# Optimization experiments

Hardware: AMD Instinct MI355X
Metric: run time of the kernel (lower is better)

## Reference

```python
import jax, jax.numpy as jnp
import numpy as np

EMBED_DIM = 1024
NUM_HEADS = 16
HEAD_DIM = EMBED_DIM // NUM_HEADS
EPS = 1e-5


def setup_inputs() -> dict:
    key = jax.random.key(0)
    ks = jax.random.split(key, 7)
    B, S, D = 4, 2048, EMBED_DIM
    s = 1.0 / np.sqrt(D)
    return {
        "x": jax.random.normal(ks[0], (B, S, D), dtype=jnp.float32),
        "W_qkv": jax.random.uniform(ks[1], (D, 3 * D), jnp.float32, -s, s),
        "b_qkv": jax.random.uniform(ks[2], (3 * D,), jnp.float32, -s, s),
        "W_out": jax.random.uniform(ks[3], (D, D), jnp.float32, -s, s),
        "b_out": jax.random.uniform(ks[4], (D,), jnp.float32, -s, s),
        "gamma": jnp.ones((D,), jnp.float32),
        "beta": jnp.zeros((D,), jnp.float32),
    }


def _layer_norm(y, gamma, beta):
    mu = jnp.mean(y, axis=-1, keepdims=True)
    var = jnp.mean(jnp.square(y - mu), axis=-1, keepdims=True)
    return (y - mu) * jax.lax.rsqrt(var + EPS) * gamma + beta


def reference(x, W_qkv, b_qkv, W_out, b_out, gamma, beta):
    B, S, D = x.shape
    H, Hd = NUM_HEADS, HEAD_DIM
    qkv = x @ W_qkv + b_qkv                       # [B,S,3D]
    q, k, v = jnp.split(qkv, 3, axis=-1)
    q = q.reshape(B, S, H, Hd).transpose(0, 2, 1, 3)  # [B,H,S,Hd]
    k = k.reshape(B, S, H, Hd).transpose(0, 2, 1, 3)
    v = v.reshape(B, S, H, Hd).transpose(0, 2, 1, 3)
    scale = 1.0 / np.sqrt(Hd)
    scores = jnp.einsum("bhsd,bhtd->bhst", q, k) * scale  # [B,H,S,S]
    attn = jax.nn.softmax(scores, axis=-1)
    ctx = jnp.einsum("bhst,bhtd->bhsd", attn, v)  # [B,H,S,Hd]
    ctx = ctx.transpose(0, 2, 1, 3).reshape(B, S, D)
    out = ctx @ W_out + b_out
    return _layer_norm(out + x, gamma, beta)
```

## Files before the change

kernel.cpp:

```cpp
#include <hip/hip_runtime.h>
#include <stdint.h>
#include <stddef.h>


#define SEQ    2048
#define DMODEL 1024
#define NHEAD  16
#define HDIM   64

typedef __attribute__((ext_vector_type(4))) float f32x4;
typedef __attribute__((ext_vector_type(16))) float f32x16;
typedef __attribute__((ext_vector_type(8))) short bf16x8;
typedef __attribute__((ext_vector_type(2))) unsigned uint2v;

static __device__ __forceinline__ unsigned short f2b(float f) {
  union { float f; unsigned u; } c; c.f = f;
  unsigned r = c.u + 0x7FFFu + ((c.u >> 16) & 1u);
  return (unsigned short)(r >> 16);
}
static __device__ __forceinline__ unsigned pkbf(float lo, float hi_) {
  unsigned r;
  asm("v_cvt_pk_bf16_f32 %0, %1, %2" : "=v"(r) : "v"(lo), "v"(hi_));
  return r;
}
static __device__ __forceinline__ float exp2v(float x) {
  return __builtin_amdgcn_exp2f(x);
}
static __device__ __forceinline__ uint2v swap32(unsigned a, unsigned b) {
  return __builtin_amdgcn_permlane32_swap(a, b, false, false);
}
static __device__ __forceinline__ void gl_lds16(const void* g, void* l) {
  __builtin_amdgcn_global_load_lds((const __attribute__((address_space(1))) void*)g,
                                   (__attribute__((address_space(3))) void*)l, 16, 0, 0);
}
static __device__ __forceinline__ int swz(int row, int col) {
  return (row * 64 + col) ^ ((row & 7) << 3);
}

__global__ __launch_bounds__(256) void k_prep(const float* __restrict__ Wqkv,
                                              const float* __restrict__ Wout,
                                              const float* __restrict__ X,
                                              unsigned short* __restrict__ wqkvT,
                                              unsigned short* __restrict__ woutT,
                                              unsigned short* __restrict__ Xb) {
  __shared__ unsigned short tile[32][33];
  const int bid = blockIdx.x;
  const int t = threadIdx.x;
  if (bid < 4096) {
    const float* in; unsigned short* out; int C, bx, by;
    if (bid < 3072) { in = Wqkv; out = wqkvT; C = 3072; bx = bid % 96; by = bid / 96; }
    else { int b2 = bid - 3072; in = Wout; out = woutT; C = 1024; bx = b2 & 31; by = b2 >> 5; }
    const int R = 1024;
    const int c0 = bx * 32, r0 = by * 32;
    const int tx = t & 31, ty = t >> 5;
#pragma unroll
    for (int j = 0; j < 4; j++) {
      int rr = ty + j * 8;
      tile[rr][tx] = f2b(in[(size_t)(r0 + rr) * C + c0 + tx]);
    }
    __syncthreads();
#pragma unroll
    for (int j = 0; j < 4; j++) {
      int rr = ty + j * 8;
      out[(size_t)(c0 + rr) * R + r0 + tx] = tile[tx][rr];
    }
  } else {
    const size_t i = ((size_t)(bid - 4096) * 256 + t) * 8;
    f32x4 a = *(const f32x4*)&X[i];
    f32x4 b = *(const f32x4*)&X[i + 4];
    bf16x8 o;
    o[0] = (short)f2b(a[0]); o[1] = (short)f2b(a[1]);
    o[2] = (short)f2b(a[2]); o[3] = (short)f2b(a[3]);
    o[4] = (short)f2b(b[0]); o[5] = (short)f2b(b[1]);
    o[6] = (short)f2b(b[2]); o[7] = (short)f2b(b[3]);
    *(bf16x8*)&Xb[i] = o;
  }
}

__global__ __launch_bounds__(256) void k_gemm_qkv(const unsigned short* __restrict__ X,
                                                  const unsigned short* __restrict__ WT,
                                                  const float* __restrict__ bias,
                                                  unsigned short* __restrict__ qb,
                                                  unsigned short* __restrict__ kb,
                                                  unsigned short* __restrict__ vt) {
  __shared__ __align__(16) unsigned short As[128 * 32];
  __shared__ __align__(16) unsigned short Bs[128 * 32];
  const int t = threadIdx.x;
  const int w = t >> 6, l = t & 63, g = l >> 4, r = l & 15;
  const int wr = w >> 1, wc = w & 1;
  const int bm = blockIdx.x * 128;
  const int bn = blockIdx.y * 128;

  f32x4 acc[4][4];
#pragma unroll
  for (int a = 0; a < 4; a++)
#pragma unroll
    for (int b = 0; b < 4; b++) acc[a][b] = f32x4{0.f, 0.f, 0.f, 0.f};

  for (int k0 = 0; k0 < DMODEL; k0 += 32) {
    __syncthreads();
#pragma unroll
    for (int j = 0; j < 2; j++) {
      int idx = t + j * 256;
      int row = idx >> 2, kc = idx & 3;
      gl_lds16(X + (size_t)(bm + row) * DMODEL + k0 + kc * 8, (char*)As + idx * 16);
      gl_lds16(WT + (size_t)(bn + row) * DMODEL + k0 + kc * 8, (char*)Bs + idx * 16);
    }
    __syncthreads();
    bf16x8 af[4], bf[4];
#pragma unroll
    for (int mf = 0; mf < 4; mf++)
      af[mf] = *(const bf16x8*)&As[(wr * 64 + mf * 16 + r) * 32 + g * 8];
#pragma unroll
    for (int nf = 0; nf < 4; nf++)
      bf[nf] = *(const bf16x8*)&Bs[(wc * 64 + nf * 16 + r) * 32 + g * 8];
#pragma unroll
    for (int mf = 0; mf < 4; mf++)
#pragma unroll
      for (int nf = 0; nf < 4; nf++)
        acc[mf][nf] = __builtin_amdgcn_mfma_f32_16x16x32_bf16(af[mf], bf[nf], acc[mf][nf], 0, 0, 0);
  }

  if (blockIdx.y >= 16) {
    __syncthreads();
    const int bi = bm >> 11, sbase = bm & 2047;
    const int h  = ((bn - 2048) >> 6) + wc;
    const int bh = bi * NHEAD + h;
    unsigned short* Ls = (w < 2) ? (As + w * 2048) : (Bs + (w - 2) * 2048);
#pragma unroll
    for (int p = 0; p < 2; p++) {
#pragma unroll
      for (int nfp = 0; nfp < 2; nfp++)
#pragma unroll
        for (int mf = 0; mf < 4; mf++)
#pragma unroll
          for (int i = 0; i < 4; i++) {
            const int nf = 2 * p + nfp;
            const int dd = nfp * 16 + r;
            const int ss = mf * 16 + g * 4 + i;
            float v = acc[mf][nf][i] + bias[bn + wc * 64 + nf * 16 + r];
            Ls[dd * 64 + (((ss >> 3) ^ (dd & 7)) * 8) + (ss & 7)] = f2b(v);
          }
#pragma unroll
      for (int j = 0; j < 4; j++) {
        const int dd = l >> 1;
        const int ch = (l & 1) * 4 + j;
        bf16x8 ov = *(const bf16x8*)&Ls[dd * 64 + ((ch ^ (dd & 7)) * 8)];
        *(bf16x8*)&vt[((size_t)bh * HDIM + 32 * p + dd) * SEQ + sbase + wr * 64 + ch * 8] = ov;
      }
    }
  } else {
#pragma unroll
    for (int mf = 0; mf < 4; mf++)
#pragma unroll
      for (int nf = 0; nf < 4; nf++)
#pragma unroll
        for (int i = 0; i < 4; i++) {
          int m = bm + wr * 64 + mf * 16 + g * 4 + i;
          int n = bn + wc * 64 + nf * 16 + r;
          float v = acc[mf][nf][i] + bias[n];
          int part = n >> 10, rem = n & 1023, h = rem >> 6, d = rem & 63;
          int bi = m >> 11, s = m & 2047;
          int bh = bi * NHEAD + h;
          if (part == 0)      qb[((size_t)bh * SEQ + s) * HDIM + d] = f2b(v * 0.18033688f);
          else                kb[((size_t)bh * SEQ + s) * HDIM + d] = f2b(v);
        }
  }
}

__global__ __launch_bounds__(256) void k_attn(const unsigned short* __restrict__ qb,
                                              const unsigned short* __restrict__ kb,
                                              const unsigned short* __restrict__ vt,
                                              unsigned short* __restrict__ ctx) {
  __shared__ __align__(16) unsigned short Qs[128 * 64];
  __shared__ __align__(16) unsigned short K0[64 * 64];
  __shared__ __align__(16) unsigned short V0[64 * 64];
  const int t = threadIdx.x;
  const int w = t >> 6, l = t & 63;
  const int ql = l & 31, hi = l >> 5;
  const int bid = blockIdx.x;
  const int xcd = bid & 7;
  const int j_  = bid >> 3;
  const int bh  = xcd * 8 + (j_ >> 4);
  const int q0  = (j_ & 15) * 128;
  const size_t qoff = ((size_t)bh * SEQ + q0) * HDIM;

#pragma unroll
  for (int j = 0; j < 4; j++) {
    int idx = t + j * 256;
    int row = idx >> 3, s = idx & 7;
    gl_lds16(qb + qoff + (size_t)row * 64 + (s ^ (row & 7)) * 8, (char*)Qs + idx * 16);
  }
#pragma unroll
  for (int j = 0; j < 2; j++) {
    int idx = t + j * 256;
    int row = idx >> 3, s = idx & 7;
    gl_lds16(kb + ((size_t)bh * SEQ + row) * HDIM + (s ^ (row & 7)) * 8, (char*)K0 + idx * 16);
    gl_lds16(vt + ((size_t)bh * HDIM + row) * SEQ + (s ^ (row & 7)) * 8, (char*)V0 + idx * 16);
  }
  asm volatile("s_waitcnt vmcnt(4)" ::: "memory");
  __builtin_amdgcn_sched_barrier(0);
  __builtin_amdgcn_s_barrier();

  bf16x8 qf[4];
#pragma unroll
  for (int ds = 0; ds < 4; ds++)
    qf[ds] = *(const bf16x8*)&Qs[swz(w * 32 + ql, ds * 16 + hi * 8)];
  asm volatile("s_waitcnt lgkmcnt(0)" ::: "memory");
  __builtin_amdgcn_sched_barrier(0);
  __builtin_amdgcn_s_barrier();

  bf16x8 ones;
#pragma unroll
  for (int i = 0; i < 8; i++) ones[i] = (short)0x3F80;

  f32x16 acc_o[2];
  f32x16 acc_l;
#pragma unroll
  for (int db = 0; db < 2; db++)
#pragma unroll
    for (int i = 0; i < 16; i++) acc_o[db][i] = 0.f;
#pragma unroll
  for (int i = 0; i < 16; i++) acc_l[i] = 0.f;

  for (int it = 0; it < SEQ / 64; ++it) {
    const int b = it & 1;
    if (it + 1 < SEQ / 64) {
      const int kt = (it + 1) * 64;
      unsigned short* Kd = (b ^ 1) ? Qs : K0;
      unsigned short* Vd = (b ^ 1) ? (Qs + 4096) : V0;
#pragma unroll
      for (int j = 0; j < 2; j++) {
        int idx = t + j * 256;
        int row = idx >> 3, s = idx & 7;
        gl_lds16(kb + ((size_t)bh * SEQ + kt + row) * HDIM + (s ^ (row & 7)) * 8,
                 (char*)Kd + idx * 16);
        gl_lds16(vt + ((size_t)bh * HDIM + row) * SEQ + kt + (s ^ (row & 7)) * 8,
                 (char*)Vd + idx * 16);
      }
      asm volatile("s_waitcnt vmcnt(4)" ::: "memory");
    } else {
      asm volatile("s_waitcnt vmcnt(0)" ::: "memory");
    }
    __builtin_amdgcn_sched_barrier(0);
    __builtin_amdgcn_s_barrier();

    const unsigned short* Kb = b ? Qs : K0;
    const unsigned short* Vb = b ? (Qs + 4096) : V0;

    bf16x8 kf[2][4];
#pragma unroll
    for (int kb2 = 0; kb2 < 2; kb2++)
#pragma unroll
      for (int ds = 0; ds < 4; ds++)
        kf[kb2][ds] = *(const bf16x8*)&Kb[swz(kb2 * 32 + ql, ds * 16 + hi * 8)];

    f32x16 accs[2];
#pragma unroll
    for (int kb2 = 0; kb2 < 2; kb2++)
#pragma unroll
      for (int i = 0; i < 16; i++) accs[kb2][i] = 0.f;
    __builtin_amdgcn_s_setprio(1);
#pragma unroll
    for (int ds = 0; ds < 4; ds++)
#pragma unroll
      for (int kb2 = 0; kb2 < 2; kb2++)
        accs[kb2] = __builtin_amdgcn_mfma_f32_32x32x16_bf16(kf[kb2][ds], qf[ds], accs[kb2], 0, 0, 0);
    __builtin_amdgcn_s_setprio(0);

#pragma unroll
    for (int kb2 = 0; kb2 < 2; kb2++)
#pragma unroll
      for (int i = 0; i < 16; i++) accs[kb2][i] = exp2v(accs[kb2][i]);

    bf16x8 pa[4];
#pragma unroll
    for (int ks = 0; ks < 4; ks++) {
      const int kb2 = ks >> 1, rb = (ks & 1) * 8;
      unsigned wA0 = pkbf(accs[kb2][rb + 0], accs[kb2][rb + 1]);
      unsigned wA1 = pkbf(accs[kb2][rb + 2], accs[kb2][rb + 3]);
      unsigned wB0 = pkbf(accs[kb2][rb + 4], accs[kb2][rb + 5]);
      unsigned wB1 = pkbf(accs[kb2][rb + 6], accs[kb2][rb + 7]);
      uint2v s0 = swap32(wB0, wA0);
      uint2v s1 = swap32(wB1, wA1);
      union { bf16x8 v; unsigned u[4]; } fr;
      fr.u[0] = s0[1]; fr.u[1] = s1[1]; fr.u[2] = s0[0]; fr.u[3] = s1[0];
      pa[ks] = fr.v;
    }

    bf16x8 vf[2][4];
#pragma unroll
    for (int db = 0; db < 2; db++)
#pragma unroll
      for (int ks = 0; ks < 4; ks++)
        vf[db][ks] = *(const bf16x8*)&Vb[swz(db * 32 + ql, ks * 16 + hi * 8)];

    __builtin_amdgcn_s_setprio(1);
#pragma unroll
    for (int ks = 0; ks < 4; ks++) {
#pragma unroll
      for (int db = 0; db < 2; db++)
        acc_o[db] = __builtin_amdgcn_mfma_f32_32x32x16_bf16(vf[db][ks], pa[ks], acc_o[db], 0, 0, 0);
      acc_l = __builtin_amdgcn_mfma_f32_32x32x16_bf16(ones, pa[ks], acc_l, 0, 0, 0);
    }
    __builtin_amdgcn_s_setprio(0);

    __builtin_amdgcn_s_barrier();
  }

  const int bi = bh >> 4, h = bh & 15;
  const float rl = 1.f / acc_l[0];
  unsigned short* Ls = Qs + w * 2048;
#pragma unroll
  for (int db = 0; db < 2; db++)
#pragma unroll
    for (int j = 0; j < 8; j++) {
      const int d0 = db * 32 + (j & 1) * 2 + (j >> 1) * 8 + hi * 4;
      *(unsigned*)&Ls[(ql * 64 + d0) ^ ((ql & 7) << 3)] =
          pkbf(acc_o[db][2 * j] * rl, acc_o[db][2 * j + 1] * rl);
    }
#pragma unroll
  for (int rq = 0; rq < 4; rq++) {
    const int q = rq * 8 + (l >> 3);
    const int c8 = l & 7;
    bf16x8 ov = *(const bf16x8*)&Ls[(q * 64 + c8 * 8) ^ ((q & 7) << 3)];
    *(bf16x8*)&ctx[((size_t)bi * SEQ + q0 + w * 32 + q) * DMODEL + h * 64 + c8 * 8] = ov;
  }
}

__global__ __launch_bounds__(256) void k_gemm_out(const unsigned short* __restrict__ A,
                                                  const unsigned short* __restrict__ WT,
                                                  const float* __restrict__ bias,
                                                  const float* __restrict__ X,
                                                  float* __restrict__ Y) {
  __shared__ __align__(16) unsigned short As[128 * 32];
  __shared__ __align__(16) unsigned short Bs[128 * 32];
  const int t = threadIdx.x;
  const int w = t >> 6, l = t & 63, g = l >> 4, r = l & 15;
  const int wr = w >> 1, wc = w & 1;
  const int bm = blockIdx.x * 128;
  const int bn = blockIdx.y * 128;

  f32x4 acc[4][4];
#pragma unroll
  for (int a = 0; a < 4; a++)
#pragma unroll
    for (int b = 0; b < 4; b++) acc[a][b] = f32x4{0.f, 0.f, 0.f, 0.f};

  for (int k0 = 0; k0 < DMODEL; k0 += 32) {
    __syncthreads();
#pragma unroll
    for (int j = 0; j < 2; j++) {
      int idx = t + j * 256;
      int row = idx >> 2, kc = idx & 3;
      gl_lds16(A + (size_t)(bm + row) * DMODEL + k0 + kc * 8, (char*)As + idx * 16);
      gl_lds16(WT + (size_t)(bn + row) * DMODEL + k0 + kc * 8, (char*)Bs + idx * 16);
    }
    __syncthreads();
    bf16x8 af[4], bf[4];
#pragma unroll
    for (int mf = 0; mf < 4; mf++)
      af[mf] = *(const bf16x8*)&As[(wr * 64 + mf * 16 + r) * 32 + g * 8];
#pragma unroll
    for (int nf = 0; nf < 4; nf++)
      bf[nf] = *(const bf16x8*)&Bs[(wc * 64 + nf * 16 + r) * 32 + g * 8];
#pragma unroll
    for (int mf = 0; mf < 4; mf++)
#pragma unroll
      for (int nf = 0; nf < 4; nf++)
        acc[mf][nf] = __builtin_amdgcn_mfma_f32_16x16x32_bf16(af[mf], bf[nf], acc[mf][nf], 0, 0, 0);
  }

#pragma unroll
  for (int mf = 0; mf < 4; mf++)
#pragma unroll
    for (int nf = 0; nf < 4; nf++)
#pragma unroll
      for (int i = 0; i < 4; i++) {
        int m = bm + wr * 64 + mf * 16 + g * 4 + i;
        int n = bn + wc * 64 + nf * 16 + r;
        float v = acc[mf][nf][i] + bias[n] + X[(size_t)m * DMODEL + n];
        Y[(size_t)m * DMODEL + n] = v;
      }
}

__global__ __launch_bounds__(256) void k_ln(const float* __restrict__ Y,
                                            const float* __restrict__ gamma,
                                            const float* __restrict__ beta,
                                            float* __restrict__ out) {
  const int row = blockIdx.x, t = threadIdx.x;
  const float* y = Y + (size_t)row * DMODEL;
  f32x4 v = *(const f32x4*)&y[t * 4];
  float s = v[0] + v[1] + v[2] + v[3];
  float q = v[0] * v[0] + v[1] * v[1] + v[2] * v[2] + v[3] * v[3];
#pragma unroll
  for (int m = 1; m < 64; m <<= 1) { s += __shfl_xor(s, m); q += __shfl_xor(q, m); }
  __shared__ float ss[4], sq[4];
  const int w = t >> 6, l = t & 63;
  if (l == 0) { ss[w] = s; sq[w] = q; }
  __syncthreads();
  s = ss[0] + ss[1] + ss[2] + ss[3];
  q = sq[0] + sq[1] + sq[2] + sq[3];
  const float mu = s * (1.f / DMODEL);
  const float var = q * (1.f / DMODEL) - mu * mu;
  const float rs = rsqrtf(var + 1e-5f);
  f32x4 o;
#pragma unroll
  for (int j = 0; j < 4; j++)
    o[j] = (v[j] - mu) * rs * gamma[t * 4 + j] + beta[t * 4 + j];
  *(f32x4*)&out[(size_t)row * DMODEL + t * 4] = o;
}

extern "C" void kernel_launch(void* const* d_in, const int* in_sizes, int n_in,
                              void* d_out, int out_size, void* d_ws, size_t ws_size,
                              hipStream_t stream) {
  const float* X     = (const float*)d_in[0];
  const float* Wqkv  = (const float*)d_in[1];
  const float* bqkv  = (const float*)d_in[2];
  const float* Wout  = (const float*)d_in[3];
  const float* bout  = (const float*)d_in[4];
  const float* gamma = (const float*)d_in[5];
  const float* beta  = (const float*)d_in[6];

  char* ws = (char*)d_ws;
  unsigned short* wqkvT = (unsigned short*)(ws);
  unsigned short* woutT = (unsigned short*)(ws + 6291456);
  unsigned short* Xb    = (unsigned short*)(ws + 8388608);
  unsigned short* ctx   = (unsigned short*)(ws + 8388608);
  unsigned short* qb    = (unsigned short*)(ws + 25165824);
  unsigned short* kb    = (unsigned short*)(ws + 41943040);
  unsigned short* vt    = (unsigned short*)(ws + 58720256);
  float*          Yf    = (float*)d_out;

  k_prep<<<dim3(8192, 1, 1), dim3(256, 1, 1), 0, stream>>>(Wqkv, Wout, X, wqkvT, woutT, Xb);
  k_gemm_qkv<<<dim3(64, 24, 1), dim3(256, 1, 1), 0, stream>>>(Xb, wqkvT, bqkv, qb, kb, vt);
  k_attn<<<dim3(1024, 1, 1), dim3(256, 1, 1), 0, stream>>>(qb, kb, vt, ctx);
  k_gemm_out<<<dim3(64, 8, 1), dim3(256, 1, 1), 0, stream>>>(ctx, woutT, bout, X, Yf);
  k_ln<<<dim3(8192, 1, 1), dim3(256, 1, 1), 0, stream>>>(Yf, gamma, beta, (float*)d_out);
}
```

Baseline: 221.5 us.

## Double attention block size to 8 waves sharing K/V tiles with dedicated buffers

The attention kernel now runs 512 threads per block covering 256 query rows, so each K/V tile loaded into LDS is shared by eight waves instead of four. K and V get their own double buffers instead of reusing the Q staging area, which removes the barrier after Q fragments are read into registers. The aim is to halve K/V global and LDS fill traffic per query row. In exchange there are half as many blocks and more LDS per block, which may lower occupancy or concurrency per CU.

```diff
diff --git a/kernel.cpp b/kernel.cpp
--- a/kernel.cpp
+++ b/kernel.cpp
@@ -168,37 +168,37 @@
   }
 }
 
-__global__ __launch_bounds__(256) void k_attn(const unsigned short* __restrict__ qb,
+__global__ __launch_bounds__(512) void k_attn(const unsigned short* __restrict__ qb,
                                               const unsigned short* __restrict__ kb,
                                               const unsigned short* __restrict__ vt,
                                               unsigned short* __restrict__ ctx) {
-  __shared__ __align__(16) unsigned short Qs[128 * 64];
+  __shared__ __align__(16) unsigned short Qs[256 * 64];
   __shared__ __align__(16) unsigned short K0[64 * 64];
+  __shared__ __align__(16) unsigned short K1[64 * 64];
   __shared__ __align__(16) unsigned short V0[64 * 64];
+  __shared__ __align__(16) unsigned short V1[64 * 64];
   const int t = threadIdx.x;
   const int w = t >> 6, l = t & 63;
   const int ql = l & 31, hi = l >> 5;
   const int bid = blockIdx.x;
   const int xcd = bid & 7;
   const int j_  = bid >> 3;
-  const int bh  = xcd * 8 + (j_ >> 4);
-  const int q0  = (j_ & 15) * 128;
+  const int bh  = xcd * 8 + (j_ >> 3);
+  const int q0  = (j_ & 7) * 256;
   const size_t qoff = ((size_t)bh * SEQ + q0) * HDIM;
 
 #pragma unroll
   for (int j = 0; j < 4; j++) {
-    int idx = t + j * 256;
+    int idx = t + j * 512;
     int row = idx >> 3, s = idx & 7;
     gl_lds16(qb + qoff + (size_t)row * 64 + (s ^ (row & 7)) * 8, (char*)Qs + idx * 16);
   }
-#pragma unroll
-  for (int j = 0; j < 2; j++) {
-    int idx = t + j * 256;
-    int row = idx >> 3, s = idx & 7;
-    gl_lds16(kb + ((size_t)bh * SEQ + row) * HDIM + (s ^ (row & 7)) * 8, (char*)K0 + idx * 16);
-    gl_lds16(vt + ((size_t)bh * HDIM + row) * SEQ + (s ^ (row & 7)) * 8, (char*)V0 + idx * 16);
-  }
-  asm volatile("s_waitcnt vmcnt(4)" ::: "memory");
+  {
+    int row = t >> 3, s = t & 7;
+    gl_lds16(kb + ((size_t)bh * SEQ + row) * HDIM + (s ^ (row & 7)) * 8, (char*)K0 + t * 16);
+    gl_lds16(vt + ((size_t)bh * HDIM + row) * SEQ + (s ^ (row & 7)) * 8, (char*)V0 + t * 16);
+  }
+  asm volatile("s_waitcnt vmcnt(2)" ::: "memory");
   __builtin_amdgcn_sched_barrier(0);
   __builtin_amdgcn_s_barrier();
 
@@ -207,8 +207,6 @@
   for (int ds = 0; ds < 4; ds++)
     qf[ds] = *(const bf16x8*)&Qs[swz(w * 32 + ql, ds * 16 + hi * 8)];
   asm volatile("s_waitcnt lgkmcnt(0)" ::: "memory");
-  __builtin_amdgcn_sched_barrier(0);
-  __builtin_amdgcn_s_barrier();
 
   bf16x8 ones;
 #pragma unroll
@@ -227,26 +225,24 @@
     const int b = it & 1;
     if (it + 1 < SEQ / 64) {
       const int kt = (it + 1) * 64;
-      unsigned short* Kd = (b ^ 1) ? Qs : K0;
-      unsigned short* Vd = (b ^ 1) ? (Qs + 4096) : V0;
-#pragma unroll
-      for (int j = 0; j < 2; j++) {
-        int idx = t + j * 256;
-        int row = idx >> 3, s = idx & 7;
+      unsigned short* Kd = b ? K0 : K1;
+      unsigned short* Vd = b ? V0 : V1;
+      {
+        int row = t >> 3, s = t & 7;
         gl_lds16(kb + ((size_t)bh * SEQ + kt + row) * HDIM + (s ^ (row & 7)) * 8,
-                 (char*)Kd + idx * 16);
+                 (char*)Kd + t * 16);
         gl_lds16(vt + ((size_t)bh * HDIM + row) * SEQ + kt + (s ^ (row & 7)) * 8,
-                 (char*)Vd + idx * 16);
+                 (char*)Vd + t * 16);
       }
-      asm volatile("s_waitcnt vmcnt(4)" ::: "memory");
+      asm volatile("s_waitcnt vmcnt(2)" ::: "memory");
     } else {
       asm volatile("s_waitcnt vmcnt(0)" ::: "memory");
     }
     __builtin_amdgcn_sched_barrier(0);
     __builtin_amdgcn_s_barrier();
 
-    const unsigned short* Kb = b ? Qs : K0;
-    const unsigned short* Vb = b ? (Qs + 4096) : V0;
+    const unsigned short* Kb = b ? K1 : K0;
+    const unsigned short* Vb = b ? V1 : V0;
 
     bf16x8 kf[2][4];
 #pragma unroll
@@ -434,7 +430,7 @@
 
   k_prep<<<dim3(8192, 1, 1), dim3(256, 1, 1), 0, stream>>>(Wqkv, Wout, X, wqkvT, woutT, Xb);
   k_gemm_qkv<<<dim3(64, 24, 1), dim3(256, 1, 1), 0, stream>>>(Xb, wqkvT, bqkv, qb, kb, vt);
-  k_attn<<<dim3(1024, 1, 1), dim3(256, 1, 1), 0, stream>>>(qb, kb, vt, ctx);
+  k_attn<<<dim3(512, 1, 1), dim3(512, 1, 1), 0, stream>>>(qb, kb, vt, ctx);
   k_gemm_out<<<dim3(64, 8, 1), dim3(256, 1, 1), 0, stream>>>(ctx, woutT, bout, X, Yf);
   k_ln<<<dim3(8192, 1, 1), dim3(256, 1, 1), 0, stream>>>(Yf, gamma, beta, (float*)d_out);
 }
```

New measurement: 208.5 us. -5.9%, faster.
